# Kernel tuning notes

Measured on AMD Instinct MI355X. Metric: run time of the kernel, lower is better.

Reference implementation:

```python
import jax, jax.numpy as jnp
import numpy as np

B, P, T = 4096, 16, 8
IN_DIM, OUT_DIM, K = 128, 128, 2
N_TABLE = 100000


def setup_inputs() -> dict:
    key = jax.random.key(0)
    ks = jax.random.split(key, 8)
    return {
        "path_input": jax.random.randint(ks[0], (B, P, T), 0, N_TABLE, dtype=jnp.int32),
        "path_num": P,
        "timestamp": T,
        "path_type": jax.random.randint(ks[1], (T,), 0, 4, dtype=jnp.int32),
        "user_emb": jax.random.normal(ks[2], (N_TABLE, IN_DIM), jnp.float32),
        "item_emb": jax.random.normal(ks[3], (N_TABLE, IN_DIM), jnp.float32),
        "ca_emb": jax.random.normal(ks[4], (N_TABLE, IN_DIM), jnp.float32),
        "ci_emb": jax.random.normal(ks[5], (N_TABLE, IN_DIM), jnp.float32),
        "conv_w": jax.random.normal(ks[6], (OUT_DIM, IN_DIM, K), jnp.float32) * 0.05,
        "conv_b": jax.random.normal(ks[7], (OUT_DIM,), jnp.float32) * 0.05,
    }


def reference(path_input, path_num, timestamp, path_type,
              user_emb, item_emb, ca_emb, ci_emb, conv_w, conv_b):
    b, p, t = path_input.shape
    # [4, N, D] stacked tables; per-position table selection via path_type
    tables = jnp.stack([user_emb, item_emb, ca_emb, ci_emb])
    # emb: [B, P, T, D]  (advanced indexing: path_type broadcasts over B, P)
    emb = tables[path_type[None, None, :], path_input]
    # conv1d over time: [B*P, D, T] -> [B*P, out, T-K+1]
    x = emb.reshape(b * p, t, -1).transpose(0, 2, 1)
    y = jax.lax.conv_general_dilated(
        x, conv_w, window_strides=(1,), padding='VALID',
        dimension_numbers=('NCH', 'OIH', 'NCH')) + conv_b[None, :, None]
    # max-pool over time, then over paths (dropout is identity in eval)
    y = y.max(axis=-1).reshape(b, p, -1)  # [B, P, out]
    return y.max(axis=1)  # [B, out]
```

## Files before the change

### kernel.cpp

```cpp
#include <hip/hip_runtime.h>

#define NB   4096
#define NBLK 256
#define NJ   16

typedef __attribute__((ext_vector_type(4))) float f32x4;
typedef __attribute__((ext_vector_type(8))) short short8;
typedef __attribute__((ext_vector_type(4))) int   int4v;

union Frag { int4v i; short8 s; };

__device__ __forceinline__ unsigned short f2bf(float f) {
  unsigned int u = __float_as_uint(f);
  u = (u + 0x7FFFu + ((u >> 16) & 1u)) >> 16;
  return (unsigned short)u;
}

__global__ __launch_bounds__(512)
void wconv_kernel(const float* __restrict__ conv_w, unsigned short* __restrict__ ws)
{
  int flat = blockIdx.x * 512 + threadIdx.x;
  int lane = flat & 63;
  int ng   = (flat >> 6) & 7;
  int ker  = (flat >> 9) & 1;
  int kk   = flat >> 10;
  int col  = ng * 16 + (lane & 15);
  int k0   = kk * 32 + (lane >> 4) * 8;
  short8 s;
#pragma unroll
  for (int j = 0; j < 8; ++j)
    s[j] = (short)f2bf(conv_w[col * 256 + (k0 + j) * 2 + ker]);
  *(short8*)(ws + (size_t)flat * 8) = s;
}

#define A0_OFF  0
#define A1_OFF  65536
#define RED_OFF 131072
#define IDX_OFF 132096
#define PTR_OFF 140288
#define LDS_BYTES 140352

__global__ __launch_bounds__(512, 2)
void path_emb_kernel(const int* __restrict__ path_input,
                     const int* __restrict__ path_type,
                     const float* __restrict__ t0, const float* __restrict__ t1,
                     const float* __restrict__ t2, const float* __restrict__ t3,
                     const unsigned short* __restrict__ wfrag,
                     const float* __restrict__ conv_b,
                     float* __restrict__ out)
{
  __shared__ __align__(16) char lds[LDS_BYTES];
  const int blk  = blockIdx.x;
  const int tid  = threadIdx.x;
  const int wid  = tid >> 6;
  const int lane = tid & 63;
  const int lrow = lane & 15;
  const int lk   = lane >> 4;
  const int R = wid & 1;
  const int C = wid >> 1;

  {
    const int4v* src = (const int4v*)(path_input + (size_t)blk * NJ * 128);
    ((int4v*)(lds + IDX_OFF))[tid] = src[tid];
  }
  if (tid < 8) {
    int ty = path_type[tid];
    const float* tb = (ty == 0) ? t0 : (ty == 1) ? t1 : (ty == 2) ? t2 : t3;
    ((const float**)(lds + PTR_OFF))[tid] = tb;
  }
  float cb = (tid < 128) ? conv_b[tid] : 0.0f;
  __syncthreads();

  auto STAGE = [&](int bufoff, int j) {
    const int* idxl = (const int*)(lds + IDX_OFF) + j * 128;
    const float* const* ptr8 = (const float* const*)(lds + PTR_OFF);
#pragma unroll
    for (int i = 0; i < 8; ++i) {
      int r0  = wid * 16 + 2 * i;
      int row = r0 + (lane >> 5);
      int idx = idxl[row];
      const float* tb = ptr8[row & 7];
      int u = lane & 31;
      const float* g = tb + (size_t)idx * 128 + ((u ^ (row & 7)) * 4);
      char* ldst = lds + bufoff + r0 * 512;
      __builtin_amdgcn_global_load_lds(
          (const __attribute__((address_space(1))) unsigned int*)g,
          (__attribute__((address_space(3))) unsigned int*)ldst, 16, 0, 0);
    }
  };

  Frag wreg[4][2][2];
#pragma unroll
  for (int kk = 0; kk < 4; ++kk)
#pragma unroll
    for (int ker = 0; ker < 2; ++ker)
#pragma unroll
      for (int n = 0; n < 2; ++n) {
        int f = (kk * 2 + ker) * 8 + C * 2 + n;
        wreg[kk][ker][n].i = *(const int4v*)(wfrag + (size_t)f * 512 + lane * 8);
      }

  STAGE(A0_OFF, 0);
  __syncthreads();

  float* red = (float*)(lds + RED_OFF);

  for (int j = 0; j < NJ; ++j) {
    const int bufc = (j & 1) ? A1_OFF : A0_OFF;
    const int bufn = (j & 1) ? A0_OFF : A1_OFF;
    if (j + 1 < NJ) STAGE(bufn, j + 1);

    f32x4 accA[4][2] = {};
    f32x4 accB[4][2] = {};
    const char* Ab = lds + bufc;
#pragma unroll
    for (int kk = 0; kk < 4; ++kk) {
      Frag a[4];
#pragma unroll
      for (int m = 0; m < 4; ++m) {
        int r  = R * 64 + m * 16 + lrow;
        int u0 = kk * 8 + lk * 2;
        int s  = r & 7;
        f32x4 e0 = *(const f32x4*)(Ab + r * 512 + ((u0 ^ s) * 16));
        f32x4 e1 = *(const f32x4*)(Ab + r * 512 + (((u0 + 1) ^ s) * 16));
        int b0, b1, b2, b3;
        asm("v_cvt_pk_bf16_f32 %0, %1, %2" : "=v"(b0) : "v"(e0[0]), "v"(e0[1]));
        asm("v_cvt_pk_bf16_f32 %0, %1, %2" : "=v"(b1) : "v"(e0[2]), "v"(e0[3]));
        asm("v_cvt_pk_bf16_f32 %0, %1, %2" : "=v"(b2) : "v"(e1[0]), "v"(e1[1]));
        asm("v_cvt_pk_bf16_f32 %0, %1, %2" : "=v"(b3) : "v"(e1[2]), "v"(e1[3]));
        int4v vi; vi[0] = b0; vi[1] = b1; vi[2] = b2; vi[3] = b3;
        a[m].i = vi;
      }
#pragma unroll
      for (int m = 0; m < 4; ++m)
#pragma unroll
        for (int n = 0; n < 2; ++n) {
          accA[m][n] = __builtin_amdgcn_mfma_f32_16x16x32_bf16(
              a[m].s, wreg[kk][0][n].s, accA[m][n], 0, 0, 0);
          accB[m][n] = __builtin_amdgcn_mfma_f32_16x16x32_bf16(
              a[m].s, wreg[kk][1][n].s, accB[m][n], 0, 0, 0);
        }
    }

    float vmax[2] = {-1e30f, -1e30f};
#pragma unroll
    for (int m = 0; m < 4; ++m)
#pragma unroll
      for (int n = 0; n < 2; ++n) {
        float up = __shfl_down(accB[m][n][0], 16);
#pragma unroll
        for (int r = 0; r < 4; ++r) {
          int rloc = lk * 4 + r;
          if ((rloc & 7) == 7) continue;
          float y2 = (r < 3) ? accB[m][n][r + 1] : up;
          vmax[n] = fmaxf(vmax[n], accA[m][n][r] + y2);
        }
      }
#pragma unroll
    for (int n = 0; n < 2; ++n) {
      float v = vmax[n];
      v = fmaxf(v, __shfl_xor(v, 16));
      v = fmaxf(v, __shfl_xor(v, 32));
      vmax[n] = v;
    }
    if (lane < 16) {
#pragma unroll
      for (int n = 0; n < 2; ++n)
        red[R * 128 + C * 32 + n * 16 + lane] = vmax[n];
    }

    asm volatile("s_waitcnt lgkmcnt(0)" ::: "memory");
    __builtin_amdgcn_sched_barrier(0);
    __builtin_amdgcn_s_barrier();
    __builtin_amdgcn_sched_barrier(0);

    if (tid < 128) {
      volatile float* rv = red;
      float m = fmaxf(rv[tid], rv[128 + tid]) + cb;
      out[(size_t)(blk * NJ + j) * 128 + tid] = m;
    }

    __syncthreads();
  }
}

extern "C" void kernel_launch(void* const* d_in, const int* in_sizes, int n_in,
                              void* d_out, int out_size, void* d_ws, size_t ws_size,
                              hipStream_t stream) {
  const int*   path_input = (const int*)d_in[0];
  const int*   path_type  = (const int*)d_in[3];
  const float* user_emb   = (const float*)d_in[4];
  const float* item_emb   = (const float*)d_in[5];
  const float* ca_emb     = (const float*)d_in[6];
  const float* ci_emb     = (const float*)d_in[7];
  const float* conv_w     = (const float*)d_in[8];
  const float* conv_b     = (const float*)d_in[9];
  float* out = (float*)d_out;
  unsigned short* wfrag = (unsigned short*)d_ws;

  wconv_kernel<<<dim3(8), dim3(512), 0, stream>>>(conv_w, wfrag);
  path_emb_kernel<<<dim3(NBLK), dim3(512), 0, stream>>>(
      path_input, path_type, user_emb, item_emb, ca_emb, ci_emb,
      wfrag, conv_b, out);
}
```

Baseline: 56.16 us.

## Stage gathered rows as bf16 via registers and defer per-row output reduction

Embedding rows are now gathered with plain global loads into registers and prefetched one step ahead. They are converted to bf16 once and written to a padded LDS buffer, replacing the direct global-to-LDS fp32 copies that were converted on every fragment read. The padded stride replaces the XOR swizzle. This halves LDS buffer size and moves the conversion off the MFMA path. Per-step partial maxima are kept in LDS and combined with the bias in a single vectorized epilogue, which drops the extra barrier and small store in each iteration. The cost is more live registers for the prefetch and a register round trip instead of an asynchronous LDS load.

```diff
diff --git a/kernel.cpp b/kernel.cpp
--- a/kernel.cpp
+++ b/kernel.cpp
@@ -14,6 +14,12 @@
   unsigned int u = __float_as_uint(f);
   u = (u + 0x7FFFu + ((u >> 16) & 1u)) >> 16;
   return (unsigned short)u;
+}
+
+__device__ __forceinline__ int cvtpk(float lo, float hi) {
+  int r;
+  asm("v_cvt_pk_bf16_f32 %0, %1, %2" : "=v"(r) : "v"(lo), "v"(hi));
+  return r;
 }
 
 __global__ __launch_bounds__(512)
@@ -34,11 +40,12 @@
 }
 
 #define A0_OFF  0
-#define A1_OFF  65536
-#define RED_OFF 131072
-#define IDX_OFF 132096
-#define PTR_OFF 140288
-#define LDS_BYTES 140352
+#define A1_OFF  34816
+#define RED_OFF 69632
+#define IDX_OFF 86016
+#define PTR_OFF 94208
+#define LDS_BYTES 94272
+#define A_STRIDE 272
 
 __global__ __launch_bounds__(512, 2)
 void path_emb_kernel(const int* __restrict__ path_input,
@@ -59,35 +66,13 @@
   const int R = wid & 1;
   const int C = wid >> 1;
 
-  {
-    const int4v* src = (const int4v*)(path_input + (size_t)blk * NJ * 128);
-    ((int4v*)(lds + IDX_OFF))[tid] = src[tid];
-  }
+  ((int4v*)(lds + IDX_OFF))[tid] =
+      ((const int4v*)(path_input + (size_t)blk * NJ * 128))[tid];
   if (tid < 8) {
     int ty = path_type[tid];
     const float* tb = (ty == 0) ? t0 : (ty == 1) ? t1 : (ty == 2) ? t2 : t3;
     ((const float**)(lds + PTR_OFF))[tid] = tb;
   }
-  float cb = (tid < 128) ? conv_b[tid] : 0.0f;
-  __syncthreads();
-
-  auto STAGE = [&](int bufoff, int j) {
-    const int* idxl = (const int*)(lds + IDX_OFF) + j * 128;
-    const float* const* ptr8 = (const float* const*)(lds + PTR_OFF);
-#pragma unroll
-    for (int i = 0; i < 8; ++i) {
-      int r0  = wid * 16 + 2 * i;
-      int row = r0 + (lane >> 5);
-      int idx = idxl[row];
-      const float* tb = ptr8[row & 7];
-      int u = lane & 31;
-      const float* g = tb + (size_t)idx * 128 + ((u ^ (row & 7)) * 4);
-      char* ldst = lds + bufoff + r0 * 512;
-      __builtin_amdgcn_global_load_lds(
-          (const __attribute__((address_space(1))) unsigned int*)g,
-          (__attribute__((address_space(3))) unsigned int*)ldst, 16, 0, 0);
-    }
-  };
 
   Frag wreg[4][2][2];
 #pragma unroll
@@ -99,16 +84,49 @@
         int f = (kk * 2 + ker) * 8 + C * 2 + n;
         wreg[kk][ker][n].i = *(const int4v*)(wfrag + (size_t)f * 512 + lane * 8);
       }
-
-  STAGE(A0_OFF, 0);
   __syncthreads();
 
+  const int grow = tid >> 2;
+  const int gq   = tid & 3;
+
+  auto ISSUE = [&](int j, f32x4 (&ld)[8]) {
+    int idx = ((const int*)(lds + IDX_OFF))[j * 128 + grow];
+    const float* tb = ((const float* const*)(lds + PTR_OFF))[grow & 7];
+    const float* g  = tb + (size_t)idx * 128 + gq * 32;
+#pragma unroll
+    for (int i = 0; i < 8; ++i) ld[i] = *(const f32x4*)(g + i * 4);
+  };
+  auto WRITE = [&](int bufoff, const f32x4 (&ld)[8]) {
+    char* dst = lds + bufoff + grow * A_STRIDE + gq * 64;
+#pragma unroll
+    for (int i = 0; i < 4; ++i) {
+      int4v w;
+      w[0] = cvtpk(ld[2 * i][0], ld[2 * i][1]);
+      w[1] = cvtpk(ld[2 * i][2], ld[2 * i][3]);
+      w[2] = cvtpk(ld[2 * i + 1][0], ld[2 * i + 1][1]);
+      w[3] = cvtpk(ld[2 * i + 1][2], ld[2 * i + 1][3]);
+      *(int4v*)(dst + i * 16) = w;
+    }
+  };
+
+  {
+    f32x4 ld0[8];
+    ISSUE(0, ld0);
+    WRITE(A0_OFF, ld0);
+  }
+  __syncthreads();
+
   float* red = (float*)(lds + RED_OFF);
+  const int arow0 = R * 64 + lrow;
 
   for (int j = 0; j < NJ; ++j) {
     const int bufc = (j & 1) ? A1_OFF : A0_OFF;
     const int bufn = (j & 1) ? A0_OFF : A1_OFF;
-    if (j + 1 < NJ) STAGE(bufn, j + 1);
+    const bool pf  = (j + 1 < NJ);
+
+    f32x4 ld[8];
+    if (pf) ISSUE(j + 1, ld);
+    __builtin_amdgcn_sched_barrier(0);
 
     f32x4 accA[4][2] = {};
     f32x4 accB[4][2] = {};
@@ -117,20 +135,8 @@
     for (int kk = 0; kk < 4; ++kk) {
       Frag a[4];
 #pragma unroll
-      for (int m = 0; m < 4; ++m) {
-        int r  = R * 64 + m * 16 + lrow;
-        int u0 = kk * 8 + lk * 2;
-        int s  = r & 7;
-        f32x4 e0 = *(const f32x4*)(Ab + r * 512 + ((u0 ^ s) * 16));
-        f32x4 e1 = *(const f32x4*)(Ab + r * 512 + (((u0 + 1) ^ s) * 16));
-        int b0, b1, b2, b3;
-        asm("v_cvt_pk_bf16_f32 %0, %1, %2" : "=v"(b0) : "v"(e0[0]), "v"(e0[1]));
-        asm("v_cvt_pk_bf16_f32 %0, %1, %2" : "=v"(b1) : "v"(e0[2]), "v"(e0[3]));
-        asm("v_cvt_pk_bf16_f32 %0, %1, %2" : "=v"(b2) : "v"(e1[0]), "v"(e1[1]));
-        asm("v_cvt_pk_bf16_f32 %0, %1, %2" : "=v"(b3) : "v"(e1[2]), "v"(e1[3]));
-        int4v vi; vi[0] = b0; vi[1] = b1; vi[2] = b2; vi[3] = b3;
-        a[m].i = vi;
-      }
+      for (int m = 0; m < 4; ++m)
+        a[m].i = *(const int4v*)(Ab + (arow0 + m * 16) * A_STRIDE + kk * 64 + lk * 16);
 #pragma unroll
       for (int m = 0; m < 4; ++m)
 #pragma unroll
@@ -166,21 +172,25 @@
     if (lane < 16) {
 #pragma unroll
       for (int n = 0; n < 2; ++n)
-        red[R * 128 + C * 32 + n * 16 + lane] = vmax[n];
-    }
-
-    asm volatile("s_waitcnt lgkmcnt(0)" ::: "memory");
-    __builtin_amdgcn_sched_barrier(0);
-    __builtin_amdgcn_s_barrier();
-    __builtin_amdgcn_sched_barrier(0);
-
-    if (tid < 128) {
-      volatile float* rv = red;
-      float m = fmaxf(rv[tid], rv[128 + tid]) + cb;
-      out[(size_t)(blk * NJ + j) * 128 + tid] = m;
-    }
-
+        red[R * (NJ * 128) + j * 128 + C * 32 + n * 16 + lane] = vmax[n];
+    }
+
+    if (pf) WRITE(bufn, ld);
     __syncthreads();
+  }
+
+  {
+    const int j  = tid >> 5;
+    const int c0 = (tid & 31) * 4;
+    const float* redA = (const float*)(lds + RED_OFF);
+    const float* redB = redA + NJ * 128;
+    f32x4 va = *(const f32x4*)(redA + j * 128 + c0);
+    f32x4 vb = *(const f32x4*)(redB + j * 128 + c0);
+    f32x4 bb = *(const f32x4*)(conv_b + c0);
+    f32x4 o;
+#pragma unroll
+    for (int k = 0; k < 4; ++k) o[k] = fmaxf(va[k], vb[k]) + bb[k];
+    *(f32x4*)(out + (size_t)(blk * NJ + j) * 128 + c0) = o;
   }
 }
 
```

New measurement: 52.54 us. 1.07x faster.
